# Performance work log

Hardware: AMD Instinct MI355X
Metric: run time of the kernel (lower is better)

## Reference

```python
import jax, jax.numpy as jnp
import numpy as np

B, C, L = 2048, 9605, 8
ALPHA = 0.5        # self.alpha
ALPHA1 = 0.05      # margin
ALPHA2 = 2.0       # asymmetric scale when violated
ALPHA3 = 5.0       # logistic sharpness
ALPHA_OTHER = 0.3  # floor on top-k threshold
TOPK = 16          # x_sorted[15] -> 16th largest


def setup_inputs() -> dict:
    key = jax.random.key(0)
    k1, k2, k3, k4 = jax.random.split(key, 4)
    x = jax.random.normal(k1, (B, C), dtype=jnp.float32)
    # each class assigned to one of 5*L slots; slots < L are whitelist groups,
    # the rest are 'other' classes (like total_indices in the torch code)
    gid = jax.random.randint(k4, (C,), 0, 5 * L)
    gid = gid.at[:L].set(jnp.arange(L))  # guarantee every group is non-empty
    group_mask = gid[None, :] == jnp.arange(L)[:, None]  # [L, C] bool
    # sparse multi-label binarized targets (~14 positives/sample)
    y = (jax.random.uniform(k2, (B, C)) < 0.0015).astype(jnp.float32)
    y_neg = (jax.random.uniform(k3, (B, C)) < 0.0015).astype(jnp.float32)
    return {"x": x, "y": y, "y_neg": y_neg, "group_mask": group_mask}


def _rank_loss(x1, x2):
    # our_rank_loss: sigmoid(alpha3*(x2-x1+margin)), scaled by alpha2 when violated
    d = x2 - x1 + ALPHA1
    s = jax.nn.sigmoid(ALPHA3 * d)
    return jnp.where(d > 0, ALPHA2 * s, s)


def reference(x, y, y_neg, group_mask):
    xs = jax.nn.sigmoid(x)  # [B, C]
    # top_k_thres = max(16th-largest sigmoid score, alpha_other)
    thres = jnp.maximum(jax.lax.top_k(xs, TOPK)[0][:, TOPK - 1], ALPHA_OTHER)  # [B]
    maskf = group_mask.astype(xs.dtype)  # [L, C]
    neg_inf = jnp.array(-jnp.inf, xs.dtype)
    # per-sample max score inside each whitelist group: [B, L]
    group_max = jnp.max(jnp.where(group_mask[None, :, :], xs[:, None, :], neg_inf), axis=-1)
    # find_gt_whitelist: group is 'hit' if any positive target inside it
    gt = (y @ maskf.T) > 0        # [B, L]
    gt_neg = (y_neg @ maskf.T) > 0  # [B, L]
    has_gt = jnp.any(gt, axis=-1)    # [B]; False <=> sentinel len(all_labels)
    has_neg = jnp.any(gt_neg, axis=-1)
    # ---- case B: sample hits at least one whitelist group ----
    rl_correct = _rank_loss(group_max, thres[:, None])    # gt groups above thres
    rl_incorrect = _rank_loss(thres[:, None], group_max)  # non-gt groups below thres
    caseB = jnp.sum(jnp.where(gt, rl_correct, rl_incorrect), axis=-1)  # [B]
    # ---- case A: no whitelist group hit ----
    union = jnp.any(group_mask, axis=0)  # [C] union of all whitelist classes
    union_max = jnp.max(jnp.where(union[None, :], xs, neg_inf), axis=-1)  # [B]
    neg_max = jnp.max(jnp.where(gt_neg, group_max, neg_inf), axis=-1)
    neg_score = jnp.where(has_neg, neg_max, jnp.zeros((), xs.dtype))  # torch starts at 0
    caseA = (1.0 - ALPHA) * _rank_loss(thres, union_max) + ALPHA * _rank_loss(thres, neg_score)
    loss_rank_all = jnp.where(has_gt, caseB, caseA)  # [B]
    return jnp.mean(loss_rank_all)
```

## Files before the change

### kernel.cpp

```cpp
#include <hip/hip_runtime.h>
#include <math.h>

constexpr int B_ = 2048;
constexpr int C_ = 9605;
constexpr int L_ = 8;
constexpr int TOPK_ = 16;
constexpr int CAPQ_ = 384;
constexpr float T0_ = 2.0f;
constexpr int CS_ = 9632;

__device__ __forceinline__ float sigm(float v) { return 1.0f / (1.0f + expf(-v)); }

__device__ __forceinline__ float rank_loss(float x1, float x2) {
  float d = x2 - x1 + 0.05f;
  float s = 1.0f / (1.0f + expf(-5.0f * d));
  return (d > 0.0f) ? 2.0f * s : s;
}

__device__ __forceinline__ unsigned int fkey(float v) {
  unsigned int u = __float_as_uint(v);
  return u ^ ((u & 0x80000000u) ? 0xFFFFFFFFu : 0x80000000u);
}
__device__ __forceinline__ float fkeyinv(unsigned int k) {
  unsigned int u = (k & 0x80000000u) ? (k ^ 0x80000000u) : ~k;
  return __uint_as_float(u);
}

__global__ void setup_kernel(const int* __restrict__ mask,
                             unsigned char* __restrict__ code4,
                             unsigned int* __restrict__ gtG,
                             unsigned int* __restrict__ gtnG) {
  const int tid = blockIdx.x * 256 + threadIdx.x;
  if (tid < CS_ + 3) {
    unsigned char cd = 0xFF;
    if (tid < C_) {
#pragma unroll
      for (int l = L_ - 1; l >= 0; --l)
        if (mask[l * C_ + tid] != 0) cd = (unsigned char)l;
    }
#pragma unroll
    for (int ld = 0; ld < 4; ++ld) {
      int p = tid - ld;
      if (p >= 0 && p < CS_) code4[ld * CS_ + p] = cd;
    }
  }
  if (tid < B_) { gtG[tid] = 0u; gtnG[tid] = 0u; }
}

__global__ void __launch_bounds__(256, 8) rows3_kernel(
    const float* __restrict__ x, const float* __restrict__ y,
    const float* __restrict__ yn, const unsigned char* __restrict__ code4,
    unsigned int* __restrict__ gslotG, unsigned int* __restrict__ gtG,
    unsigned int* __restrict__ gtnG, float* __restrict__ x16G) {
  __shared__ unsigned int slots[256 * 9];
  __shared__ float4 cand4[CAPQ_];
  __shared__ int cnt;
  __shared__ float s_x16;
  __shared__ int s_flag, s_red;
  __shared__ unsigned int wb[4];

  const int g = (int)blockIdx.x >> 11;
  const int r = (int)blockIdx.x & 2047;
  const int t = threadIdx.x;
  const int lead = (4 - ((r * C_) & 3)) & 3;
  const int n4 = (C_ - lead) >> 2;
  const size_t rowb = (size_t)r * C_;

  if (g == 0) {
#pragma unroll
    for (int i = 0; i < 9; ++i) slots[t * 9 + i] = 0u;
    if (t == 0) { cnt = 0; s_flag = 0; }
    __syncthreads();

    const float* xb = x + rowb + lead;
    const unsigned int* cb = (const unsigned int*)(code4 + (size_t)lead * CS_);

#pragma unroll
    for (int k = 0; k < 10; ++k) {
      const int j = t + (k << 8);
      if (j < n4) {
        float4 X = *reinterpret_cast<const float4*>(xb + (j << 2));
        unsigned int cw = cb[j];
        {
          unsigned int k0 = (X.x > 0.0f) ? (__float_as_uint(X.x) | 0x80000000u) : 0u;
          unsigned int k1 = (X.y > 0.0f) ? (__float_as_uint(X.y) | 0x80000000u) : 0u;
          unsigned int k2 = (X.z > 0.0f) ? (__float_as_uint(X.z) | 0x80000000u) : 0u;
          unsigned int k3 = (X.w > 0.0f) ? (__float_as_uint(X.w) | 0x80000000u) : 0u;
          unsigned int a0 = min(cw & 0xFFu, 8u);
          unsigned int a1 = min((cw >> 8) & 0xFFu, 8u);
          unsigned int a2 = min((cw >> 16) & 0xFFu, 8u);
          unsigned int a3 = min(cw >> 24, 8u);
          atomicMax(&slots[t * 9 + a0], k0);
          atomicMax(&slots[t * 9 + a1], k1);
          atomicMax(&slots[t * 9 + a2], k2);
          atomicMax(&slots[t * 9 + a3], k3);
        }
        float mx = fmaxf(fmaxf(X.x, X.y), fmaxf(X.z, X.w));
        if (mx > T0_) {
          int p = atomicAdd(&cnt, 1);
          if (p < CAPQ_) cand4[p] = X;
        }
      }
    }

    if (t < 4) {
      auto sc = [&](int c) {
        float xv = x[rowb + c];
        unsigned int cd = code4[c];
        unsigned int key = (xv > 0.0f) ? (__float_as_uint(xv) | 0x80000000u) : 0u;
        atomicMax(&slots[t * 9 + min(cd, 8u)], key);
        if (xv > T0_) {
          int p = atomicAdd(&cnt, 1);
          if (p < CAPQ_) cand4[p] = make_float4(xv, -INFINITY, -INFINITY, -INFINITY);
        }
      };
      if (t < lead) sc(t);
      int c2 = lead + (n4 << 2) + t;
      if (c2 < C_) sc(c2);
    }
    __syncthreads();

    for (int s = 128; s > 0; s >>= 1) {
      if (t < s) {
#pragma unroll
        for (int l = 0; l < 8; ++l) {
          unsigned int o = slots[(t + s) * 9 + l];
          if (o > slots[t * 9 + l]) slots[t * 9 + l] = o;
        }
      }
      __syncthreads();
    }
    if (t < 8) gslotG[r * 8 + t] = slots[t];

    const int qn = cnt;
    const bool ok_path = (qn >= 4) && (qn <= CAPQ_);
    if (ok_path && t < 64) {
      const float* cf = reinterpret_cast<const float*>(cand4);
      const int nvv = qn << 2;
      unsigned int ku[CAPQ_ * 4 / 64];
#pragma unroll
      for (int k = 0; k < CAPQ_ * 4 / 64; ++k) {
        int i = t + (k << 6);
        ku[k] = (i < nvv) ? fkey(cf[i]) : 0u;
      }
      unsigned int lo = 0u, hi = 0xFFFFFFFFu;
#pragma unroll 1
      for (int it = 0; it < 32 && lo < hi; ++it) {
        unsigned int mid = lo + ((hi - lo) >> 1) + 1u;
        int c16 = 0;
#pragma unroll
        for (int k = 0; k < CAPQ_ * 4 / 64; ++k) c16 += (ku[k] >= mid) ? 1 : 0;
#pragma unroll
        for (int off = 32; off > 0; off >>= 1) c16 += __shfl_xor(c16, off, 64);
        if (c16 >= TOPK_) lo = mid; else hi = mid - 1u;
      }
      if (t == 0) {
        float v = fkeyinv(lo);
        s_x16 = v;
        s_flag = (v > T0_) ? 1 : 0;
      }
    }
    __syncthreads();
    if (!(ok_path && s_flag != 0)) {
      const float* xr = x + rowb;
      unsigned int lo = 0u, hi = 0xFFFFFFFFu;
      for (int it = 0; it < 32; ++it) {
        if (lo >= hi) break;
        unsigned int mid = lo + ((hi - lo) >> 1) + 1u;
        if (t == 0) s_red = 0;
        __syncthreads();
        int cl = 0;
        for (int c = t; c < C_; c += 256) cl += (fkey(xr[c]) >= mid) ? 1 : 0;
        atomicAdd(&s_red, cl);
        __syncthreads();
        int total = s_red;
        __syncthreads();
        if (total >= TOPK_) lo = mid; else hi = mid - 1u;
      }
      if (t == 0) s_x16 = fkeyinv(lo);
    }
    __syncthreads();
    if (t == 0) x16G[r] = s_x16;
  } else {
    const float* src = (g == 1) ? y : yn;
    unsigned int* dst = (g == 1) ? gtG : gtnG;
    const float* sb = src + rowb + lead;
    unsigned int bits = 0u;

#pragma unroll
    for (int k = 0; k < 10; ++k) {
      const int j = t + (k << 8);
      if (j < n4) {
        float4 V = *reinterpret_cast<const float4*>(sb + (j << 2));
        if (V.x > 0.0f || V.y > 0.0f || V.z > 0.0f || V.w > 0.0f) {
          int c = lead + (j << 2);
          if (V.x > 0.0f) { unsigned int cd = code4[c];     if (cd < 8u) bits |= 1u << cd; }
          if (V.y > 0.0f) { unsigned int cd = code4[c + 1]; if (cd < 8u) bits |= 1u << cd; }
          if (V.z > 0.0f) { unsigned int cd = code4[c + 2]; if (cd < 8u) bits |= 1u << cd; }
          if (V.w > 0.0f) { unsigned int cd = code4[c + 3]; if (cd < 8u) bits |= 1u << cd; }
        }
      }
    }
    if (t < 4) {
      if (t < lead) {
        float v = src[rowb + t];
        if (v > 0.0f) { unsigned int cd = code4[t]; if (cd < 8u) bits |= 1u << cd; }
      }
      int c2 = lead + (n4 << 2) + t;
      if (c2 < C_) {
        float v = src[rowb + c2];
        if (v > 0.0f) { unsigned int cd = code4[c2]; if (cd < 8u) bits |= 1u << cd; }
      }
    }
#pragma unroll
    for (int off = 32; off > 0; off >>= 1) bits |= __shfl_xor(bits, off, 64);
    if ((t & 63) == 0) wb[t >> 6] = bits;
    __syncthreads();
    if (t == 0) dst[r] = wb[0] | wb[1] | wb[2] | wb[3];
  }
}

__global__ void finish_kernel(const unsigned int* __restrict__ gslotG,
                              const unsigned int* __restrict__ gtG,
                              const unsigned int* __restrict__ gtnG,
                              const float* __restrict__ x16G,
                              float* __restrict__ loss) {
  const int r = blockIdx.x * 256 + threadIdx.x;
  if (r >= B_) return;
  float thres = fmaxf(sigm(x16G[r]), 0.3f);
  unsigned int gtb = gtG[r], gnb = gtnG[r];
  float caseB = 0.0f, unio = -INFINITY, negmax = -INFINITY;
#pragma unroll
  for (int l = 0; l < L_; ++l) {
    float gm = __uint_as_float(gslotG[r * L_ + l] ^ 0x80000000u);
    float g = sigm(gm);
    unio = fmaxf(unio, g);
    caseB += ((gtb >> l) & 1u) ? rank_loss(g, thres) : rank_loss(thres, g);
    if ((gnb >> l) & 1u) negmax = fmaxf(negmax, g);
  }
  float negscore = (gnb != 0u) ? negmax : 0.0f;
  float caseA = 0.5f * rank_loss(thres, unio) + 0.5f * rank_loss(thres, negscore);
  loss[r] = (gtb != 0u) ? caseB : caseA;
}

__global__ void mean_kernel(const float* __restrict__ loss, float* __restrict__ out) {
  const int t = threadIdx.x;
  float s = 0.0f;
  for (int i = t; i < B_; i += 256) s += loss[i];
#pragma unroll
  for (int off = 32; off > 0; off >>= 1) s += __shfl_xor(s, off, 64);
  __shared__ float part[4];
  if ((t & 63) == 0) part[t >> 6] = s;
  __syncthreads();
  if (t == 0) out[0] = (part[0] + part[1] + part[2] + part[3]) * (1.0f / (float)B_);
}

extern "C" void kernel_launch(void* const* d_in, const int* in_sizes, int n_in,
                              void* d_out, int out_size, void* d_ws, size_t ws_size,
                              hipStream_t stream) {
  const float* x = (const float*)d_in[0];
  const float* y = (const float*)d_in[1];
  const float* yn = (const float*)d_in[2];
  const int* mask = (const int*)d_in[3];

  constexpr size_t OFF_LOSS = 0;
  constexpr size_t OFF_CODE4 = 8192;
  constexpr size_t OFF_GSLOT = OFF_CODE4 + 4 * CS_;
  constexpr size_t OFF_GT = OFF_GSLOT + B_ * L_ * 4;
  constexpr size_t OFF_GTN = OFF_GT + B_ * 4;
  constexpr size_t OFF_X16 = OFF_GTN + B_ * 4;

  float* loss = (float*)((char*)d_ws + OFF_LOSS);
  unsigned char* code4 = (unsigned char*)d_ws + OFF_CODE4;
  unsigned int* gslotG = (unsigned int*)((char*)d_ws + OFF_GSLOT);
  unsigned int* gtG = (unsigned int*)((char*)d_ws + OFF_GT);
  unsigned int* gtnG = (unsigned int*)((char*)d_ws + OFF_GTN);
  float* x16G = (float*)((char*)d_ws + OFF_X16);

  hipLaunchKernelGGL(setup_kernel, dim3(38), dim3(256), 0, stream,
                     mask, code4, gtG, gtnG);
  hipLaunchKernelGGL(rows3_kernel, dim3(3 * B_), dim3(256), 0, stream,
                     x, y, yn, code4, gslotG, gtG, gtnG, x16G);
  hipLaunchKernelGGL(finish_kernel, dim3((B_ + 255) / 256), dim3(256), 0, stream,
                     gslotG, gtG, gtnG, x16G, loss);
  hipLaunchKernelGGL(mean_kernel, dim3(1), dim3(256), 0, stream,
                     loss, (float*)d_out);
}
```

Baseline: 254.8 us.

## Stage each row into LDS via global_load_lds and use shared group-max atomics

Each block now copies its whole row (x, y or y_neg) into LDS with direct global-to-LDS dword loads, then reads aligned float4s from LDS. This removes the misaligned-row handling and the four shifted copies of the class-code table. The per-thread 9-slot arrays and their tree reduction are replaced by 8 shared slots updated with guarded atomicMax. The fallback top-k search now scans LDS instead of global memory. The ~38KB LDS row limits occupancy per CU and adds a full vmcnt wait before any compute.

```diff
diff --git a/kernel.cpp b/kernel.cpp
--- a/kernel.cpp
+++ b/kernel.cpp
@@ -7,7 +7,11 @@
 constexpr int TOPK_ = 16;
 constexpr int CAPQ_ = 384;
 constexpr float T0_ = 2.0f;
-constexpr int CS_ = 9632;
+constexpr int CPAD_ = 9728;
+constexpr int NQ_ = 2401;
+constexpr int TAIL_ = 9604;
+constexpr int WCHUNK_ = 2432;
+constexpr int WQ_ = 608;
 
 __device__ __forceinline__ float sigm(float v) { return 1.0f / (1.0f + expf(-v)); }
 
@@ -26,34 +30,37 @@
   return __uint_as_float(u);
 }
 
+__device__ __forceinline__ void gld4(const float* gsrc, float* ldst) {
+  __builtin_amdgcn_global_load_lds(
+      (const __attribute__((address_space(1))) unsigned int*)gsrc,
+      (__attribute__((address_space(3))) unsigned int*)ldst, 4, 0, 0);
+}
+
 __global__ void setup_kernel(const int* __restrict__ mask,
-                             unsigned char* __restrict__ code4,
+                             unsigned char* __restrict__ code,
                              unsigned int* __restrict__ gtG,
                              unsigned int* __restrict__ gtnG) {
   const int tid = blockIdx.x * 256 + threadIdx.x;
-  if (tid < CS_ + 3) {
+  if (tid < CPAD_) {
     unsigned char cd = 0xFF;
     if (tid < C_) {
 #pragma unroll
       for (int l = L_ - 1; l >= 0; --l)
         if (mask[l * C_ + tid] != 0) cd = (unsigned char)l;
     }
-#pragma unroll
-    for (int ld = 0; ld < 4; ++ld) {
-      int p = tid - ld;
-      if (p >= 0 && p < CS_) code4[ld * CS_ + p] = cd;
-    }
+    code[tid] = cd;
   }
   if (tid < B_) { gtG[tid] = 0u; gtnG[tid] = 0u; }
 }
 
-__global__ void __launch_bounds__(256, 8) rows3_kernel(
+__global__ void __launch_bounds__(256) staged_kernel(
     const float* __restrict__ x, const float* __restrict__ y,
-    const float* __restrict__ yn, const unsigned char* __restrict__ code4,
+    const float* __restrict__ yn, const unsigned char* __restrict__ code,
     unsigned int* __restrict__ gslotG, unsigned int* __restrict__ gtG,
     unsigned int* __restrict__ gtnG, float* __restrict__ x16G) {
-  __shared__ unsigned int slots[256 * 9];
+  __shared__ __align__(16) float xs[CPAD_];
   __shared__ float4 cand4[CAPQ_];
+  __shared__ unsigned int gslot[L_];
   __shared__ int cnt;
   __shared__ float s_x16;
   __shared__ int s_flag, s_red;
@@ -62,39 +69,52 @@
   const int g = (int)blockIdx.x >> 11;
   const int r = (int)blockIdx.x & 2047;
   const int t = threadIdx.x;
-  const int lead = (4 - ((r * C_) & 3)) & 3;
-  const int n4 = (C_ - lead) >> 2;
+  const int w = t >> 6;
+  const int ln = t & 63;
   const size_t rowb = (size_t)r * C_;
+  const float* sr = ((g == 0) ? x : ((g == 1) ? y : yn)) + rowb;
+
+  if (t < L_) gslot[t] = 0u;
+  if (t == 0) { cnt = 0; s_flag = 0; }
+  __syncthreads();
+
+  const int fbase = w * WCHUNK_;
+  {
+    float* lb = &xs[fbase];
+    if (fbase + WCHUNK_ <= C_) {
+#pragma unroll
+      for (int i = 0; i < 38; ++i) gld4(sr + fbase + (i << 6) + ln, lb + (i << 6));
+    } else {
+#pragma unroll
+      for (int i = 0; i < 38; ++i) {
+        int idx = fbase + (i << 6) + ln;
+        if (idx < C_) gld4(sr + idx, lb + (i << 6));
+      }
+    }
+  }
+  asm volatile("s_waitcnt vmcnt(0)" ::: "memory");
+  __builtin_amdgcn_sched_barrier(0);
+
+  const int q0 = w * WQ_;
+  const int q1 = (q0 + WQ_ < NQ_) ? (q0 + WQ_) : NQ_;
 
   if (g == 0) {
-#pragma unroll
-    for (int i = 0; i < 9; ++i) slots[t * 9 + i] = 0u;
-    if (t == 0) { cnt = 0; s_flag = 0; }
-    __syncthreads();
-
-    const float* xb = x + rowb + lead;
-    const unsigned int* cb = (const unsigned int*)(code4 + (size_t)lead * CS_);
-
-#pragma unroll
-    for (int k = 0; k < 10; ++k) {
-      const int j = t + (k << 8);
-      if (j < n4) {
-        float4 X = *reinterpret_cast<const float4*>(xb + (j << 2));
-        unsigned int cw = cb[j];
-        {
-          unsigned int k0 = (X.x > 0.0f) ? (__float_as_uint(X.x) | 0x80000000u) : 0u;
-          unsigned int k1 = (X.y > 0.0f) ? (__float_as_uint(X.y) | 0x80000000u) : 0u;
-          unsigned int k2 = (X.z > 0.0f) ? (__float_as_uint(X.z) | 0x80000000u) : 0u;
-          unsigned int k3 = (X.w > 0.0f) ? (__float_as_uint(X.w) | 0x80000000u) : 0u;
-          unsigned int a0 = min(cw & 0xFFu, 8u);
-          unsigned int a1 = min((cw >> 8) & 0xFFu, 8u);
-          unsigned int a2 = min((cw >> 16) & 0xFFu, 8u);
-          unsigned int a3 = min(cw >> 24, 8u);
-          atomicMax(&slots[t * 9 + a0], k0);
-          atomicMax(&slots[t * 9 + a1], k1);
-          atomicMax(&slots[t * 9 + a2], k2);
-          atomicMax(&slots[t * 9 + a3], k3);
-        }
+    const unsigned int* cdw = (const unsigned int*)code;
+#pragma unroll
+    for (int i = 0; i < 10; ++i) {
+      int j = q0 + (i << 6) + ln;
+      if (j < q1) {
+        float4 X = ((const float4*)xs)[j];
+        unsigned int cw = cdw[j];
+        unsigned int cd, k;
+        cd = cw & 0xFFu;
+        if (cd < 8u && X.x > 0.0f) { k = __float_as_uint(X.x) | 0x80000000u; if (k > gslot[cd]) atomicMax(&gslot[cd], k); }
+        cd = (cw >> 8) & 0xFFu;
+        if (cd < 8u && X.y > 0.0f) { k = __float_as_uint(X.y) | 0x80000000u; if (k > gslot[cd]) atomicMax(&gslot[cd], k); }
+        cd = (cw >> 16) & 0xFFu;
+        if (cd < 8u && X.z > 0.0f) { k = __float_as_uint(X.z) | 0x80000000u; if (k > gslot[cd]) atomicMax(&gslot[cd], k); }
+        cd = cw >> 24;
+        if (cd < 8u && X.w > 0.0f) { k = __float_as_uint(X.w) | 0x80000000u; if (k > gslot[cd]) atomicMax(&gslot[cd], k); }
         float mx = fmaxf(fmaxf(X.x, X.y), fmaxf(X.z, X.w));
         if (mx > T0_) {
           int p = atomicAdd(&cnt, 1);
@@ -102,35 +122,19 @@
         }
       }
     }
-
-    if (t < 4) {
-      auto sc = [&](int c) {
-        float xv = x[rowb + c];
-        unsigned int cd = code4[c];
-        unsigned int key = (xv > 0.0f) ? (__float_as_uint(xv) | 0x80000000u) : 0u;
-        atomicMax(&slots[t * 9 + min(cd, 8u)], key);
-        if (xv > T0_) {
-          int p = atomicAdd(&cnt, 1);
-          if (p < CAPQ_) cand4[p] = make_float4(xv, -INFINITY, -INFINITY, -INFINITY);
-        }
-      };
-      if (t < lead) sc(t);
-      int c2 = lead + (n4 << 2) + t;
-      if (c2 < C_) sc(c2);
-    }
-    __syncthreads();
-
-    for (int s = 128; s > 0; s >>= 1) {
-      if (t < s) {
-#pragma unroll
-        for (int l = 0; l < 8; ++l) {
-          unsigned int o = slots[(t + s) * 9 + l];
-          if (o > slots[t * 9 + l]) slots[t * 9 + l] = o;
-        }
-      }
-      __syncthreads();
-    }
-    if (t < 8) gslotG[r * 8 + t] = slots[t];
+    if (t == 192) {
+      float xv = xs[TAIL_];
+      unsigned int cd = code[TAIL_];
+      if (cd < 8u && xv > 0.0f)
+        atomicMax(&gslot[cd], __float_as_uint(xv) | 0x80000000u);
+      if (xv > T0_) {
+        int p = atomicAdd(&cnt, 1);
+        if (p < CAPQ_) cand4[p] = make_float4(xv, -INFINITY, -INFINITY, -INFINITY);
+      }
+    }
+    __syncthreads();
+
+    if (t < 8) gslotG[r * 8 + t] = gslot[t];
 
     const int qn = cnt;
     const bool ok_path = (qn >= 4) && (qn <= CAPQ_);
@@ -162,7 +166,6 @@
     }
     __syncthreads();
     if (!(ok_path && s_flag != 0)) {
-      const float* xr = x + rowb;
       unsigned int lo = 0u, hi = 0xFFFFFFFFu;
       for (int it = 0; it < 32; ++it) {
         if (lo >= hi) break;
@@ -170,7 +173,7 @@
         if (t == 0) s_red = 0;
         __syncthreads();
         int cl = 0;
-        for (int c = t; c < C_; c += 256) cl += (fkey(xr[c]) >= mid) ? 1 : 0;
+        for (int c = t; c < C_; c += 256) cl += (fkey(xs[c]) >= mid) ? 1 : 0;
         atomicAdd(&s_red, cl);
         __syncthreads();
         int total = s_red;
@@ -182,41 +185,31 @@
     __syncthreads();
     if (t == 0) x16G[r] = s_x16;
   } else {
-    const float* src = (g == 1) ? y : yn;
-    unsigned int* dst = (g == 1) ? gtG : gtnG;
-    const float* sb = src + rowb + lead;
     unsigned int bits = 0u;
-
-#pragma unroll
-    for (int k = 0; k < 10; ++k) {
-      const int j = t + (k << 8);
-      if (j < n4) {
-        float4 V = *reinterpret_cast<const float4*>(sb + (j << 2));
+#pragma unroll
+    for (int i = 0; i < 10; ++i) {
+      int j = q0 + (i << 6) + ln;
+      if (j < q1) {
+        float4 V = ((const float4*)xs)[j];
         if (V.x > 0.0f || V.y > 0.0f || V.z > 0.0f || V.w > 0.0f) {
-          int c = lead + (j << 2);
-          if (V.x > 0.0f) { unsigned int cd = code4[c];     if (cd < 8u) bits |= 1u << cd; }
-          if (V.y > 0.0f) { unsigned int cd = code4[c + 1]; if (cd < 8u) bits |= 1u << cd; }
-          if (V.z > 0.0f) { unsigned int cd = code4[c + 2]; if (cd < 8u) bits |= 1u << cd; }
-          if (V.w > 0.0f) { unsigned int cd = code4[c + 3]; if (cd < 8u) bits |= 1u << cd; }
+          int c = j << 2;
+          if (V.x > 0.0f) { unsigned int cd = code[c];     if (cd < 8u) bits |= 1u << cd; }
+          if (V.y > 0.0f) { unsigned int cd = code[c + 1]; if (cd < 8u) bits |= 1u << cd; }
+          if (V.z > 0.0f) { unsigned int cd = code[c + 2]; if (cd < 8u) bits |= 1u << cd; }
+          if (V.w > 0.0f) { unsigned int cd = code[c + 3]; if (cd < 8u) bits |= 1u << cd; }
         }
       }
     }
-    if (t < 4) {
-      if (t < lead) {
-        float v = src[rowb + t];
-        if (v > 0.0f) { unsigned int cd = code4[t]; if (cd < 8u) bits |= 1u << cd; }
-      }
-      int c2 = lead + (n4 << 2) + t;
-      if (c2 < C_) {
-        float v = src[rowb + c2];
-        if (v > 0.0f) { unsigned int cd = code4[c2]; if (cd < 8u) bits |= 1u << cd; }
-      }
+    if (t == 192 && xs[TAIL_] > 0.0f) {
+      unsigned int cd = code[TAIL_];
+      if (cd < 8u) bits |= 1u << cd;
     }
 #pragma unroll
     for (int off = 32; off > 0; off >>= 1) bits |= __shfl_xor(bits, off, 64);
-    if ((t & 63) == 0) wb[t >> 6] = bits;
-    __syncthreads();
-    if (t == 0) dst[r] = wb[0] | wb[1] | wb[2] | wb[3];
+    if (ln == 0) wb[w] = bits;
+    __syncthreads();
+    if (t == 0)
+      ((g == 1) ? gtG : gtnG)[r] = wb[0] | wb[1] | wb[2] | wb[3];
   }
 }
 
@@ -264,23 +257,23 @@
   const int* mask = (const int*)d_in[3];
 
   constexpr size_t OFF_LOSS = 0;
-  constexpr size_t OFF_CODE4 = 8192;
-  constexpr size_t OFF_GSLOT = OFF_CODE4 + 4 * CS_;
+  constexpr size_t OFF_CODE = 8192;
+  constexpr size_t OFF_GSLOT = OFF_CODE + CPAD_;
   constexpr size_t OFF_GT = OFF_GSLOT + B_ * L_ * 4;
   constexpr size_t OFF_GTN = OFF_GT + B_ * 4;
   constexpr size_t OFF_X16 = OFF_GTN + B_ * 4;
 
   float* loss = (float*)((char*)d_ws + OFF_LOSS);
-  unsigned char* code4 = (unsigned char*)d_ws + OFF_CODE4;
+  unsigned char* code = (unsigned char*)d_ws + OFF_CODE;
   unsigned int* gslotG = (unsigned int*)((char*)d_ws + OFF_GSLOT);
   unsigned int* gtG = (unsigned int*)((char*)d_ws + OFF_GT);
   unsigned int* gtnG = (unsigned int*)((char*)d_ws + OFF_GTN);
   float* x16G = (float*)((char*)d_ws + OFF_X16);
 
   hipLaunchKernelGGL(setup_kernel, dim3(38), dim3(256), 0, stream,
-                     mask, code4, gtG, gtnG);
-  hipLaunchKernelGGL(rows3_kernel, dim3(3 * B_), dim3(256), 0, stream,
-                     x, y, yn, code4, gslotG, gtG, gtnG, x16G);
+                     mask, code, gtG, gtnG);
+  hipLaunchKernelGGL(staged_kernel, dim3(3 * B_), dim3(256), 0, stream,
+                     x, y, yn, code, gslotG, gtG, gtnG, x16G);
   hipLaunchKernelGGL(finish_kernel, dim3((B_ + 255) / 256), dim3(256), 0, stream,
                      gslotG, gtG, gtnG, x16G, loss);
   hipLaunchKernelGGL(mean_kernel, dim3(1), dim3(256), 0, stream,
```

Result: slower. 276.9 us (+8.7%).

## Flatten row sweep into grid-stride wave pass with global atomics and candidate buffer

Applied to the files above, without the earlier changes.

Replaces the per-row block reduction with a flat sweep over the whole B*C array. Each wavefront handles 256 contiguous elements, which may span two rows. Group maxima go to global atomicMax (skipped when the stored value is already larger), label bits go to global atomicOr, and candidates above the threshold are compacted through ballot and mbcnt prefix sums into a per-row global buffer. Top-k selection moves to a separate one-wave-per-row finish kernel. The aim is to remove the shared-memory slot reductions and block barriers and to balance the memory streaming, at the cost of global atomic traffic and an extra read of the candidate buffer.

```diff
diff --git a/kernel.cpp b/kernel.cpp
--- a/kernel.cpp
+++ b/kernel.cpp
@@ -5,7 +5,7 @@
 constexpr int C_ = 9605;
 constexpr int L_ = 8;
 constexpr int TOPK_ = 16;
-constexpr int CAPQ_ = 384;
+constexpr int CAPC_ = 384;
 constexpr float T0_ = 2.0f;
 constexpr int CS_ = 9632;
 
@@ -26,10 +26,18 @@
   return __uint_as_float(u);
 }
 
+__device__ __forceinline__ int mprefix(unsigned long long m) {
+  return (int)__builtin_amdgcn_mbcnt_hi(
+      (unsigned int)(m >> 32),
+      __builtin_amdgcn_mbcnt_lo((unsigned int)m, 0u));
+}
+
 __global__ void setup_kernel(const int* __restrict__ mask,
                              unsigned char* __restrict__ code4,
+                             unsigned int* __restrict__ gslotG,
                              unsigned int* __restrict__ gtG,
-                             unsigned int* __restrict__ gtnG) {
+                             unsigned int* __restrict__ gtnG,
+                             int* __restrict__ cntG) {
   const int tid = blockIdx.x * 256 + threadIdx.x;
   if (tid < CS_ + 3) {
     unsigned char cd = 0xFF;
@@ -44,203 +52,208 @@
       if (p >= 0 && p < CS_) code4[ld * CS_ + p] = cd;
     }
   }
-  if (tid < B_) { gtG[tid] = 0u; gtnG[tid] = 0u; }
-}
-
-__global__ void __launch_bounds__(256, 8) rows3_kernel(
+  for (int i = tid; i < B_ * 8; i += 9728) gslotG[i] = 0x80000000u;
+  for (int i = tid; i < B_; i += 9728) { gtG[i] = 0u; gtnG[i] = 0u; cntG[i] = 0; }
+}
+
+__global__ void __launch_bounds__(256, 8) wave_sweep(
     const float* __restrict__ x, const float* __restrict__ y,
     const float* __restrict__ yn, const unsigned char* __restrict__ code4,
     unsigned int* __restrict__ gslotG, unsigned int* __restrict__ gtG,
-    unsigned int* __restrict__ gtnG, float* __restrict__ x16G) {
-  __shared__ unsigned int slots[256 * 9];
-  __shared__ float4 cand4[CAPQ_];
-  __shared__ int cnt;
-  __shared__ float s_x16;
-  __shared__ int s_flag, s_red;
-  __shared__ unsigned int wb[4];
-
+    unsigned int* __restrict__ gtnG, int* __restrict__ cntG,
+    float* __restrict__ candG) {
+  constexpr int NE = B_ * C_;
+  constexpr int NQ = NE / 4;
+  constexpr int TTQ = 2048 * 256;
+  constexpr int NSTEP = (NQ + TTQ - 1) / TTQ;
+  const int t = threadIdx.x;
   const int g = (int)blockIdx.x >> 11;
-  const int r = (int)blockIdx.x & 2047;
+  const int vb = (int)blockIdx.x & 2047;
+  const int ln = t & 63;
+  const float* src = (g == 0) ? x : ((g == 1) ? y : yn);
+
+#pragma unroll 1
+  for (int step = 0; step < NSTEP; ++step) {
+    const int qw = step * TTQ + vb * 256 + (t & ~63);
+    if (qw >= NQ) continue;
+    const int q = qw + ln;
+    const int efirst = qw << 2;
+    const int rfirst = efirst / C_;
+    int elast = efirst + 255; if (elast >= NE) elast = NE - 1;
+    const bool single = (elast / C_) == rfirst;
+    const bool act = (q < NQ);
+
+    float4 V = make_float4(0.0f, 0.0f, 0.0f, 0.0f);
+    int e0 = 0, row = rfirst, cc = 0;
+    bool wrapq = false;
+    unsigned int cw = 0u;
+    if (act) {
+      e0 = q << 2;
+      V = *reinterpret_cast<const float4*>(src + e0);
+      row = e0 / C_;
+      cc = e0 - row * C_;
+      wrapq = (cc + 3 >= C_);
+      if (!wrapq)
+        cw = *reinterpret_cast<const unsigned int*>(
+            code4 + (size_t)(((cc & 3) * CS_) + (cc & ~3)));
+    }
+    const bool cok = act && !wrapq;
+
+    if (g == 0) {
+      if (cok) {
+        const float xv[4] = {V.x, V.y, V.z, V.w};
+#pragma unroll
+        for (int k2 = 0; k2 < 4; ++k2) {
+          unsigned int cd = (cw >> (8 * k2)) & 0xFFu;
+          float xk = xv[k2];
+          if (cd < 8u && xk > 0.0f) {
+            unsigned int key = __float_as_uint(xk) | 0x80000000u;
+            unsigned int cur = gslotG[row * 8 + (int)cd];
+            if (key > cur) atomicMax(&gslotG[row * 8 + (int)cd], key);
+          }
+        }
+      } else if (act) {
+        const float xv[4] = {V.x, V.y, V.z, V.w};
+        int ccc = cc, rw = row;
+#pragma unroll
+        for (int k2 = 0; k2 < 4; ++k2) {
+          unsigned int cd = code4[ccc];
+          float xk = xv[k2];
+          if (cd < 8u && xk > 0.0f)
+            atomicMax(&gslotG[rw * 8 + (int)cd],
+                      __float_as_uint(xk) | 0x80000000u);
+          if (xk > T0_) {
+            int p = atomicAdd(&cntG[rw], 1);
+            if (p < CAPC_) candG[(size_t)rw * CAPC_ + p] = xk;
+          }
+          if (++ccc == C_) { ccc = 0; ++rw; }
+        }
+      }
+      if (single) {
+        unsigned long long m0 = __ballot(cok && V.x > T0_);
+        unsigned long long m1 = __ballot(cok && V.y > T0_);
+        unsigned long long m2 = __ballot(cok && V.z > T0_);
+        unsigned long long m3 = __ballot(cok && V.w > T0_);
+        int n0 = __popcll(m0), n1 = __popcll(m1), n2 = __popcll(m2);
+        int tot = n0 + n1 + n2 + __popcll(m3);
+        if (tot) {
+          int base = 0;
+          if (ln == 0) base = atomicAdd(&cntG[rfirst], tot);
+          base = __shfl(base, 0, 64);
+          float* cr = candG + (size_t)rfirst * CAPC_;
+          if (cok) {
+            if (V.x > T0_) { int p = base + mprefix(m0); if (p < CAPC_) cr[p] = V.x; }
+            if (V.y > T0_) { int p = base + n0 + mprefix(m1); if (p < CAPC_) cr[p] = V.y; }
+            if (V.z > T0_) { int p = base + n0 + n1 + mprefix(m2); if (p < CAPC_) cr[p] = V.z; }
+            if (V.w > T0_) { int p = base + n0 + n1 + n2 + mprefix(m3); if (p < CAPC_) cr[p] = V.w; }
+          }
+        }
+      } else if (cok) {
+        const float xv[4] = {V.x, V.y, V.z, V.w};
+#pragma unroll
+        for (int k2 = 0; k2 < 4; ++k2) {
+          if (xv[k2] > T0_) {
+            int p = atomicAdd(&cntG[row], 1);
+            if (p < CAPC_) candG[(size_t)row * CAPC_ + p] = xv[k2];
+          }
+        }
+      }
+    } else {
+      unsigned int b0 = 0u, b1 = 0u;
+      if (cok) {
+        unsigned int bb = 0u;
+        if (V.x > 0.0f) { unsigned int cd = cw & 0xFFu;        if (cd < 8u) bb |= 1u << cd; }
+        if (V.y > 0.0f) { unsigned int cd = (cw >> 8) & 0xFFu; if (cd < 8u) bb |= 1u << cd; }
+        if (V.z > 0.0f) { unsigned int cd = (cw >> 16) & 0xFFu;if (cd < 8u) bb |= 1u << cd; }
+        if (V.w > 0.0f) { unsigned int cd = cw >> 24;          if (cd < 8u) bb |= 1u << cd; }
+        if (row == rfirst) b0 = bb; else b1 = bb;
+      } else if (act) {
+        const float xv[4] = {V.x, V.y, V.z, V.w};
+        int ccc = cc, rw = row;
+#pragma unroll
+        for (int k2 = 0; k2 < 4; ++k2) {
+          if (xv[k2] > 0.0f) {
+            unsigned int cd = code4[ccc];
+            if (cd < 8u) { if (rw == rfirst) b0 |= 1u << cd; else b1 |= 1u << cd; }
+          }
+          if (++ccc == C_) { ccc = 0; ++rw; }
+        }
+      }
+      if (__any((int)(b0 | b1))) {
+#pragma unroll
+        for (int off = 32; off > 0; off >>= 1) {
+          b0 |= __shfl_xor(b0, off, 64);
+          b1 |= __shfl_xor(b1, off, 64);
+        }
+        unsigned int* dst = (g == 1) ? gtG : gtnG;
+        if (ln == 0) {
+          if (b0) atomicOr(&dst[rfirst], b0);
+          if (b1) atomicOr(&dst[rfirst + 1], b1);
+        }
+      }
+    }
+  }
+}
+
+__global__ void finish_kernel(
+    const float* __restrict__ x, const unsigned int* __restrict__ gslotG,
+    const unsigned int* __restrict__ gtG, const unsigned int* __restrict__ gtnG,
+    const int* __restrict__ cntG, const float* __restrict__ candG,
+    float* __restrict__ loss) {
+  const int r = blockIdx.x;
   const int t = threadIdx.x;
-  const int lead = (4 - ((r * C_) & 3)) & 3;
-  const int n4 = (C_ - lead) >> 2;
-  const size_t rowb = (size_t)r * C_;
-
-  if (g == 0) {
-#pragma unroll
-    for (int i = 0; i < 9; ++i) slots[t * 9 + i] = 0u;
-    if (t == 0) { cnt = 0; s_flag = 0; }
-    __syncthreads();
-
-    const float* xb = x + rowb + lead;
-    const unsigned int* cb = (const unsigned int*)(code4 + (size_t)lead * CS_);
-
-#pragma unroll
-    for (int k = 0; k < 10; ++k) {
-      const int j = t + (k << 8);
-      if (j < n4) {
-        float4 X = *reinterpret_cast<const float4*>(xb + (j << 2));
-        unsigned int cw = cb[j];
-        {
-          unsigned int k0 = (X.x > 0.0f) ? (__float_as_uint(X.x) | 0x80000000u) : 0u;
-          unsigned int k1 = (X.y > 0.0f) ? (__float_as_uint(X.y) | 0x80000000u) : 0u;
-          unsigned int k2 = (X.z > 0.0f) ? (__float_as_uint(X.z) | 0x80000000u) : 0u;
-          unsigned int k3 = (X.w > 0.0f) ? (__float_as_uint(X.w) | 0x80000000u) : 0u;
-          unsigned int a0 = min(cw & 0xFFu, 8u);
-          unsigned int a1 = min((cw >> 8) & 0xFFu, 8u);
-          unsigned int a2 = min((cw >> 16) & 0xFFu, 8u);
-          unsigned int a3 = min(cw >> 24, 8u);
-          atomicMax(&slots[t * 9 + a0], k0);
-          atomicMax(&slots[t * 9 + a1], k1);
-          atomicMax(&slots[t * 9 + a2], k2);
-          atomicMax(&slots[t * 9 + a3], k3);
-        }
-        float mx = fmaxf(fmaxf(X.x, X.y), fmaxf(X.z, X.w));
-        if (mx > T0_) {
-          int p = atomicAdd(&cnt, 1);
-          if (p < CAPQ_) cand4[p] = X;
-        }
-      }
-    }
-
-    if (t < 4) {
-      auto sc = [&](int c) {
-        float xv = x[rowb + c];
-        unsigned int cd = code4[c];
-        unsigned int key = (xv > 0.0f) ? (__float_as_uint(xv) | 0x80000000u) : 0u;
-        atomicMax(&slots[t * 9 + min(cd, 8u)], key);
-        if (xv > T0_) {
-          int p = atomicAdd(&cnt, 1);
-          if (p < CAPQ_) cand4[p] = make_float4(xv, -INFINITY, -INFINITY, -INFINITY);
-        }
-      };
-      if (t < lead) sc(t);
-      int c2 = lead + (n4 << 2) + t;
-      if (c2 < C_) sc(c2);
-    }
-    __syncthreads();
-
-    for (int s = 128; s > 0; s >>= 1) {
-      if (t < s) {
-#pragma unroll
-        for (int l = 0; l < 8; ++l) {
-          unsigned int o = slots[(t + s) * 9 + l];
-          if (o > slots[t * 9 + l]) slots[t * 9 + l] = o;
-        }
-      }
-      __syncthreads();
-    }
-    if (t < 8) gslotG[r * 8 + t] = slots[t];
-
-    const int qn = cnt;
-    const bool ok_path = (qn >= 4) && (qn <= CAPQ_);
-    if (ok_path && t < 64) {
-      const float* cf = reinterpret_cast<const float*>(cand4);
-      const int nvv = qn << 2;
-      unsigned int ku[CAPQ_ * 4 / 64];
-#pragma unroll
-      for (int k = 0; k < CAPQ_ * 4 / 64; ++k) {
-        int i = t + (k << 6);
-        ku[k] = (i < nvv) ? fkey(cf[i]) : 0u;
-      }
-      unsigned int lo = 0u, hi = 0xFFFFFFFFu;
+  const int cnt = cntG[r];
+  float x16;
+  if (cnt >= TOPK_ && cnt <= CAPC_) {
+    const float* cf = candG + (size_t)r * CAPC_;
+    unsigned int ku[CAPC_ / 64];
+#pragma unroll
+    for (int k = 0; k < CAPC_ / 64; ++k) {
+      int i = t + (k << 6);
+      ku[k] = (i < cnt) ? fkey(cf[i]) : 0u;
+    }
+    unsigned int lo = 0u, hi = 0xFFFFFFFFu;
 #pragma unroll 1
-      for (int it = 0; it < 32 && lo < hi; ++it) {
-        unsigned int mid = lo + ((hi - lo) >> 1) + 1u;
-        int c16 = 0;
-#pragma unroll
-        for (int k = 0; k < CAPQ_ * 4 / 64; ++k) c16 += (ku[k] >= mid) ? 1 : 0;
-#pragma unroll
-        for (int off = 32; off > 0; off >>= 1) c16 += __shfl_xor(c16, off, 64);
-        if (c16 >= TOPK_) lo = mid; else hi = mid - 1u;
-      }
-      if (t == 0) {
-        float v = fkeyinv(lo);
-        s_x16 = v;
-        s_flag = (v > T0_) ? 1 : 0;
-      }
-    }
-    __syncthreads();
-    if (!(ok_path && s_flag != 0)) {
-      const float* xr = x + rowb;
-      unsigned int lo = 0u, hi = 0xFFFFFFFFu;
-      for (int it = 0; it < 32; ++it) {
-        if (lo >= hi) break;
-        unsigned int mid = lo + ((hi - lo) >> 1) + 1u;
-        if (t == 0) s_red = 0;
-        __syncthreads();
-        int cl = 0;
-        for (int c = t; c < C_; c += 256) cl += (fkey(xr[c]) >= mid) ? 1 : 0;
-        atomicAdd(&s_red, cl);
-        __syncthreads();
-        int total = s_red;
-        __syncthreads();
-        if (total >= TOPK_) lo = mid; else hi = mid - 1u;
-      }
-      if (t == 0) s_x16 = fkeyinv(lo);
-    }
-    __syncthreads();
-    if (t == 0) x16G[r] = s_x16;
+    for (int it = 0; it < 32 && lo < hi; ++it) {
+      unsigned int mid = lo + ((hi - lo) >> 1) + 1u;
+      int c16 = 0;
+#pragma unroll
+      for (int k = 0; k < CAPC_ / 64; ++k) c16 += (ku[k] >= mid) ? 1 : 0;
+#pragma unroll
+      for (int off = 32; off > 0; off >>= 1) c16 += __shfl_xor(c16, off, 64);
+      if (c16 >= TOPK_) lo = mid; else hi = mid - 1u;
+    }
+    x16 = fkeyinv(lo);
   } else {
-    const float* src = (g == 1) ? y : yn;
-    unsigned int* dst = (g == 1) ? gtG : gtnG;
-    const float* sb = src + rowb + lead;
-    unsigned int bits = 0u;
-
-#pragma unroll
-    for (int k = 0; k < 10; ++k) {
-      const int j = t + (k << 8);
-      if (j < n4) {
-        float4 V = *reinterpret_cast<const float4*>(sb + (j << 2));
-        if (V.x > 0.0f || V.y > 0.0f || V.z > 0.0f || V.w > 0.0f) {
-          int c = lead + (j << 2);
-          if (V.x > 0.0f) { unsigned int cd = code4[c];     if (cd < 8u) bits |= 1u << cd; }
-          if (V.y > 0.0f) { unsigned int cd = code4[c + 1]; if (cd < 8u) bits |= 1u << cd; }
-          if (V.z > 0.0f) { unsigned int cd = code4[c + 2]; if (cd < 8u) bits |= 1u << cd; }
-          if (V.w > 0.0f) { unsigned int cd = code4[c + 3]; if (cd < 8u) bits |= 1u << cd; }
-        }
-      }
-    }
-    if (t < 4) {
-      if (t < lead) {
-        float v = src[rowb + t];
-        if (v > 0.0f) { unsigned int cd = code4[t]; if (cd < 8u) bits |= 1u << cd; }
-      }
-      int c2 = lead + (n4 << 2) + t;
-      if (c2 < C_) {
-        float v = src[rowb + c2];
-        if (v > 0.0f) { unsigned int cd = code4[c2]; if (cd < 8u) bits |= 1u << cd; }
-      }
-    }
-#pragma unroll
-    for (int off = 32; off > 0; off >>= 1) bits |= __shfl_xor(bits, off, 64);
-    if ((t & 63) == 0) wb[t >> 6] = bits;
-    __syncthreads();
-    if (t == 0) dst[r] = wb[0] | wb[1] | wb[2] | wb[3];
+    const float* xr = x + (size_t)r * C_;
+    unsigned int lo = 0u, hi = 0xFFFFFFFFu;
+#pragma unroll 1
+    for (int it = 0; it < 32 && lo < hi; ++it) {
+      unsigned int mid = lo + ((hi - lo) >> 1) + 1u;
+      int cl = 0;
+      for (int c = t; c < C_; c += 64) cl += (fkey(xr[c]) >= mid) ? 1 : 0;
+#pragma unroll
+      for (int off = 32; off > 0; off >>= 1) cl += __shfl_xor(cl, off, 64);
+      if (cl >= TOPK_) lo = mid; else hi = mid - 1u;
+    }
+    x16 = fkeyinv(lo);
   }
-}
-
-__global__ void finish_kernel(const unsigned int* __restrict__ gslotG,
-                              const unsigned int* __restrict__ gtG,
-                              const unsigned int* __restrict__ gtnG,
-                              const float* __restrict__ x16G,
-                              float* __restrict__ loss) {
-  const int r = blockIdx.x * 256 + threadIdx.x;
-  if (r >= B_) return;
-  float thres = fmaxf(sigm(x16G[r]), 0.3f);
-  unsigned int gtb = gtG[r], gnb = gtnG[r];
-  float caseB = 0.0f, unio = -INFINITY, negmax = -INFINITY;
-#pragma unroll
-  for (int l = 0; l < L_; ++l) {
-    float gm = __uint_as_float(gslotG[r * L_ + l] ^ 0x80000000u);
-    float g = sigm(gm);
-    unio = fmaxf(unio, g);
-    caseB += ((gtb >> l) & 1u) ? rank_loss(g, thres) : rank_loss(thres, g);
-    if ((gnb >> l) & 1u) negmax = fmaxf(negmax, g);
+  if (t == 0) {
+    float thres = fmaxf(sigm(x16), 0.3f);
+    unsigned int gtb = gtG[r], gnb = gtnG[r];
+    float caseB = 0.0f, unio = -INFINITY, negmax = -INFINITY;
+#pragma unroll
+    for (int l = 0; l < L_; ++l) {
+      float gm = __uint_as_float(gslotG[r * 8 + l] ^ 0x80000000u);
+      float g = sigm(gm);
+      unio = fmaxf(unio, g);
+      caseB += ((gtb >> l) & 1u) ? rank_loss(g, thres) : rank_loss(thres, g);
+      if ((gnb >> l) & 1u) negmax = fmaxf(negmax, g);
+    }
+    float negscore = (gnb != 0u) ? negmax : 0.0f;
+    float caseA = 0.5f * rank_loss(thres, unio) + 0.5f * rank_loss(thres, negscore);
+    loss[r] = (gtb != 0u) ? caseB : caseA;
   }
-  float negscore = (gnb != 0u) ? negmax : 0.0f;
-  float caseA = 0.5f * rank_loss(thres, unio) + 0.5f * rank_loss(thres, negscore);
-  loss[r] = (gtb != 0u) ? caseB : caseA;
 }
 
 __global__ void mean_kernel(const float* __restrict__ loss, float* __restrict__ out) {
@@ -266,23 +279,25 @@
   constexpr size_t OFF_LOSS = 0;
   constexpr size_t OFF_CODE4 = 8192;
   constexpr size_t OFF_GSLOT = OFF_CODE4 + 4 * CS_;
-  constexpr size_t OFF_GT = OFF_GSLOT + B_ * L_ * 4;
+  constexpr size_t OFF_GT = OFF_GSLOT + B_ * 8 * 4;
   constexpr size_t OFF_GTN = OFF_GT + B_ * 4;
-  constexpr size_t OFF_X16 = OFF_GTN + B_ * 4;
+  constexpr size_t OFF_CNT = OFF_GTN + B_ * 4;
+  constexpr size_t OFF_CAND = OFF_CNT + B_ * 4;
 
   float* loss = (float*)((char*)d_ws + OFF_LOSS);
   unsigned char* code4 = (unsigned char*)d_ws + OFF_CODE4;
   unsigned int* gslotG = (unsigned int*)((char*)d_ws + OFF_GSLOT);
   unsigned int* gtG = (unsigned int*)((char*)d_ws + OFF_GT);
   unsigned int* gtnG = (unsigned int*)((char*)d_ws + OFF_GTN);
-  float* x16G = (float*)((char*)d_ws + OFF_X16);
+  int* cntG = (int*)((char*)d_ws + OFF_CNT);
+  float* candG = (float*)((char*)d_ws + OFF_CAND);
 
   hipLaunchKernelGGL(setup_kernel, dim3(38), dim3(256), 0, stream,
-                     mask, code4, gtG, gtnG);
-  hipLaunchKernelGGL(rows3_kernel, dim3(3 * B_), dim3(256), 0, stream,
-                     x, y, yn, code4, gslotG, gtG, gtnG, x16G);
-  hipLaunchKernelGGL(finish_kernel, dim3((B_ + 255) / 256), dim3(256), 0, stream,
-                     gslotG, gtG, gtnG, x16G, loss);
+                     mask, code4, gslotG, gtG, gtnG, cntG);
+  hipLaunchKernelGGL(wave_sweep, dim3(3 * 2048), dim3(256), 0, stream,
+                     x, y, yn, code4, gslotG, gtG, gtnG, cntG, candG);
+  hipLaunchKernelGGL(finish_kernel, dim3(2048), dim3(64), 0, stream,
+                     x, gslotG, gtG, gtnG, cntG, candG, loss);
   hipLaunchKernelGGL(mean_kernel, dim3(1), dim3(256), 0, stream,
                      loss, (float*)d_out);
 }
```

Result: slower. 370.5 us (+45.4%).
